# Optimization experiments

Hardware: AMD Instinct MI355X
Metric: run time of the kernel (lower is better)

## Reference

```python
import jax, jax.numpy as jnp
import numpy as np

V, E, H, L = 2048, 512, 1024, 2   # vocab, emb_dim, hidden, num_layers
NUM_LABELS = [50, 20, 10]
S, T = 1024, 512                   # encoder seq len, max_out_char_seq_len


def _gru_layer(xs, h0, wih, whh, bih, bhh):
    # torch GRU cell: r,z,n gate order. xs: (T, Din), h0: (H,)
    def step(h, x):
        gx = x @ wih.T + bih
        gh = h @ whh.T + bhh
        xr, xz, xn = jnp.split(gx, 3)
        hr, hz, hn = jnp.split(gh, 3)
        r = jax.nn.sigmoid(xr + hr)
        z = jax.nn.sigmoid(xz + hz)
        n = jnp.tanh(xn + r * hn)
        h_new = (1.0 - z) * n + z * h
        return h_new, h_new
    hT, hs = jax.lax.scan(step, h0, xs)
    return hs, hT


def _gru(xs, h0, params):
    # params: list of (wih, whh, bih, bhh) per layer; h0: (L, H)
    outs, finals = [], []
    inp = xs
    for l, (wih, whh, bih, bhh) in enumerate(params):
        hs, hT = _gru_layer(inp, h0[l], wih, whh, bih, bhh)
        outs.append(hs)
        finals.append(hT)
        inp = hs
    return outs, jnp.stack(finals)


def _forward(char_seq, target_char_seq, enc_state, emb,
             enc_wih0, enc_whh0, enc_bih0, enc_bhh0,
             enc_wih1, enc_whh1, enc_bih1, enc_bhh1,
             dec_wih0, dec_whh0, dec_bih0, dec_bhh0,
             dec_wih1, dec_whh1, dec_bih1, dec_bhh1,
             out_w, out_b, cls_w0, cls_b0, cls_w1, cls_b1, cls_w2, cls_b2,
             sos, max_out_char_seq_len, max_num_labels):
    enc_params = [(enc_wih0, enc_whh0, enc_bih0, enc_bhh0),
                  (enc_wih1, enc_whh1, enc_bih1, enc_bhh1)]
    dec_params = [(dec_wih0, dec_whh0, dec_bih0, dec_bhh0),
                  (dec_wih1, dec_whh1, dec_bih1, dec_bhh1)]
    # encode_: mask = char_seq != 0 is all-True by construction (inputs drawn from [4, V))
    _, h_enc = _gru(emb[char_seq], enc_state.reshape(L, H), enc_params)
    # teacher-forced decode: step t consumes <s> for t=0 else target[t-1];
    # targets contain no eos/sep, so the loop runs exactly max_out_char_seq_len steps
    dec_in = jnp.concatenate([jnp.asarray([sos], dtype=target_char_seq.dtype),
                              target_char_seq[: max_out_char_seq_len - 1]])
    layer_hs, _ = _gru(emb[dec_in], h_enc, dec_params)
    # char_dropout is identity in eval mode
    char_scores = layer_hs[-1] @ out_w.T + out_b            # (T, H) -- char_out_size == hidden
    char_scores_out = char_scores[None]                      # (1, T, H), no padding (full-length decode)
    # per-step stacked layer states, view(1, -1, L*H) layout == layer-major concat
    char_states_out = jnp.stack(layer_hs, axis=1).reshape(1, max_out_char_seq_len, L * H)
    # final decoder_label_step_ on last char_scores; padded to max_num_labels
    last = char_scores[-1]
    labels = []
    for w, b in ((cls_w0, cls_b0), (cls_w1, cls_b1), (cls_w2, cls_b2)):
        s = last @ w.T + b                                   # (num,)
        labels.append(jnp.pad(s[None, None, :], ((0, 0), (0, max_num_labels - 1), (0, 0))))
    return (char_scores_out, char_states_out, labels[0], labels[1], labels[2])


def setup_inputs() -> dict:
    key = jax.random.key(0)
    ks = list(jax.random.split(key, 40))
    nrm = lambda k, sh: jax.random.normal(k, sh, dtype=jnp.float32) * 0.05
    inp = {}
    inp["char_seq"] = jax.random.randint(ks[0], (S,), 4, V)       # avoid pad/sos/eos/sep ids
    inp["target_char_seq"] = jax.random.randint(ks[1], (T,), 4, V)
    inp["enc_state"] = nrm(ks[2], (L * H,))
    inp["emb"] = nrm(ks[3], (V, E))
    i = 4
    for pre in ("enc", "dec"):
        for l in range(L):
            din = E if l == 0 else H
            inp[f"{pre}_wih{l}"] = nrm(ks[i], (3 * H, din)); i += 1
            inp[f"{pre}_whh{l}"] = nrm(ks[i], (3 * H, H)); i += 1
            inp[f"{pre}_bih{l}"] = nrm(ks[i], (3 * H,)); i += 1
            inp[f"{pre}_bhh{l}"] = nrm(ks[i], (3 * H,)); i += 1
    inp["out_w"] = nrm(ks[i], (H, H)); i += 1
    inp["out_b"] = nrm(ks[i], (H,)); i += 1
    for j, n in enumerate(NUM_LABELS):
        inp[f"cls_w{j}"] = nrm(ks[i], (n, H)); i += 1
        inp[f"cls_b{j}"] = nrm(ks[i], (n,)); i += 1
    inp["sos"] = 1
    inp["max_out_char_seq_len"] = T
    inp["max_num_labels"] = 3
    return inp


def reference(char_seq, target_char_seq, enc_state, emb,
              enc_wih0, enc_whh0, enc_bih0, enc_bhh0,
              enc_wih1, enc_whh1, enc_bih1, enc_bhh1,
              dec_wih0, dec_whh0, dec_bih0, dec_bhh0,
              dec_wih1, dec_whh1, dec_bih1, dec_bhh1,
              out_w, out_b, cls_w0, cls_b0, cls_w1, cls_b1, cls_w2, cls_b2,
              sos, max_out_char_seq_len, max_num_labels):
    return _forward(char_seq, target_char_seq, enc_state, emb,
                    enc_wih0, enc_whh0, enc_bih0, enc_bhh0,
                    enc_wih1, enc_whh1, enc_bih1, enc_bhh1,
                    dec_wih0, dec_whh0, dec_bih0, dec_bhh0,
                    dec_wih1, dec_whh1, dec_bih1, dec_bhh1,
                    out_w, out_b, cls_w0, cls_b0, cls_w1, cls_b1, cls_w2, cls_b2,
                    sos, max_out_char_seq_len, max_num_labels)
```

## Files before the change

### kernel.cpp

```cpp
#include <hip/hip_runtime.h>
#include <hip/hip_bf16.h>
#include <cstdint>

#define Hh   1024
#define G3   3072
#define POISON_U 0xFFFFFFFFu

__device__ __forceinline__ float sigmoidf_(float x) { return 1.f / (1.f + __expf(-x)); }

__device__ __forceinline__ float ld_agent(const float* p) {
    return __hip_atomic_load(p, __ATOMIC_RELAXED, __HIP_MEMORY_SCOPE_AGENT);
}
__device__ __forceinline__ void st_agent(float* p, float v) {
    __hip_atomic_store(p, v, __ATOMIC_RELAXED, __HIP_MEMORY_SCOPE_AGENT);
}
__device__ __forceinline__ float poll_val(const float* p) {
    float v = ld_agent(p);
    int guard = 0;
    while (__float_as_uint(v) == POISON_U) {
        __builtin_amdgcn_s_sleep(1);
        v = ld_agent(p);
        if (++guard > (1 << 20)) break;
    }
    return v;
}

__global__ __launch_bounds__(128) void gather_emb(const int* __restrict__ char_seq,
    const int* __restrict__ target, const int* __restrict__ sos,
    const float* __restrict__ emb, float* __restrict__ x_enc, float* __restrict__ x_dec)
{
    const int r = blockIdx.x;
    int id; float* dst;
    if (r < 1024) { id = char_seq[r]; dst = x_enc + (size_t)r * 512; }
    else {
        const int rd = r - 1024;
        id = (rd == 0) ? sos[0] : target[rd - 1];
        dst = x_dec + (size_t)rd * 512;
    }
    const float4* src = (const float4*)(emb + (size_t)id * 512);
    ((float4*)dst)[threadIdx.x] = src[threadIdx.x];
}

__global__ __launch_bounds__(256) void gemm_nt(const float* __restrict__ A,
    const float* __restrict__ W, const float* __restrict__ bias,
    float* __restrict__ C, int M, int N, int K)
{
    __shared__ float As[16][68];
    __shared__ float Ws[16][68];
    const int tid = threadIdx.x;
    const int tx = tid & 15, ty = tid >> 4;
    const int row0 = blockIdx.y * 64, col0 = blockIdx.x * 64;
    const int lr = tid >> 2;
    const int ls = (tid & 3) << 2;
    float acc[4][4] = {};
    for (int k0 = 0; k0 < K; k0 += 16) {
        const float4 a4 = *(const float4*)(A + (size_t)(row0 + lr) * K + k0 + ls);
        const float4 w4 = *(const float4*)(W + (size_t)(col0 + lr) * K + k0 + ls);
        As[ls + 0][lr] = a4.x; As[ls + 1][lr] = a4.y; As[ls + 2][lr] = a4.z; As[ls + 3][lr] = a4.w;
        Ws[ls + 0][lr] = w4.x; Ws[ls + 1][lr] = w4.y; Ws[ls + 2][lr] = w4.z; Ws[ls + 3][lr] = w4.w;
        __syncthreads();
        #pragma unroll
        for (int k = 0; k < 16; ++k) {
            const float4 a = *(const float4*)&As[k][ty << 2];
            const float4 w = *(const float4*)&Ws[k][tx << 2];
            const float av[4] = {a.x, a.y, a.z, a.w};
            const float wv[4] = {w.x, w.y, w.z, w.w};
            #pragma unroll
            for (int i = 0; i < 4; ++i)
                #pragma unroll
                for (int j = 0; j < 4; ++j)
                    acc[i][j] += av[i] * wv[j];
        }
        __syncthreads();
    }
    const int cc = col0 + (tx << 2);
    #pragma unroll
    for (int i = 0; i < 4; ++i) {
        float4 o;
        o.x = acc[i][0] + bias[cc + 0];
        o.y = acc[i][1] + bias[cc + 1];
        o.z = acc[i][2] + bias[cc + 2];
        o.w = acc[i][3] + bias[cc + 3];
        *(float4*)(C + (size_t)(row0 + (ty << 2) + i) * N + cc) = o;
    }
}

__global__ __launch_bounds__(512, 2) void fused_gru2(
    const float* __restrict__ gx0,
    const float* __restrict__ whh0, const float* __restrict__ bhh0,
    const float* __restrict__ wih1, const float* __restrict__ bih1,
    const float* __restrict__ whh1, const float* __restrict__ bhh1,
    const float* __restrict__ h0i, const float* __restrict__ h1i,
    float* __restrict__ hs0, float* __restrict__ hs1, int S)
{
    __shared__ float sh0[Hh];
    __shared__ float sh1[Hh];
    const int tid = threadIdx.x;
    const int wg  = blockIdx.x;
    const bool isL1 = (wg >= 128);
    const int ln = tid & 63;
    const int wv = tid >> 6;
    const int uu = ((isL1 ? wg - 128 : wg) << 3) + wv;

    float4 wa[3][4], wb[3][4];
    const float* WA = isL1 ? wih1 : whh0;
    #pragma unroll
    for (int g = 0; g < 3; ++g)
        #pragma unroll
        for (int j = 0; j < 4; ++j)
            wa[g][j] = *(const float4*)(WA + (size_t)(g * Hh + uu) * Hh + ((ln + 64 * j) << 2));
    if (isL1) {
        #pragma unroll
        for (int g = 0; g < 3; ++g)
            #pragma unroll
            for (int j = 0; j < 4; ++j)
                wb[g][j] = *(const float4*)(whh1 + (size_t)(g * Hh + uu) * Hh + ((ln + 64 * j) << 2));
    } else {
        #pragma unroll
        for (int g = 0; g < 3; ++g)
            #pragma unroll
            for (int j = 0; j < 4; ++j)
                wb[g][j] = make_float4(0.f, 0.f, 0.f, 0.f);
    }
    const float* BA = isL1 ? bih1 : bhh0;
    const float ba_r = BA[uu], ba_z = BA[Hh + uu], ba_n = BA[2 * Hh + uu];
    const float bb_r = isL1 ? bhh1[uu] : 0.f;
    const float bb_z = isL1 ? bhh1[Hh + uu] : 0.f;
    const float bb_n = isL1 ? bhh1[2 * Hh + uu] : 0.f;

    const float4* s0f4 = (const float4*)sh0;
    const float4* s1f4 = (const float4*)sh1;

    for (int t = 0; t < S; ++t) {
        float xr = 0.f, xz = 0.f, xn = 0.f;
        if (!isL1 && ln == 0) {
            const float* gxt = gx0 + (size_t)t * G3 + uu;
            xr = gxt[0]; xz = gxt[Hh]; xn = gxt[2 * Hh];
        }

        if (!isL1) {
            if (t == 0) {
                sh0[tid] = h0i[tid]; sh0[tid + 512] = h0i[tid + 512];
            } else {
                const float* row = hs0 + (size_t)t * Hh;
                const float v0 = poll_val(&row[tid]);
                const float v1 = poll_val(&row[tid + 512]);
                sh0[tid] = v0; sh0[tid + 512] = v1;
            }
        } else {
            const float* rx = hs0 + (size_t)(t + 1) * Hh;
            const float v0 = poll_val(&rx[tid]);
            const float v1 = poll_val(&rx[tid + 512]);
            sh0[tid] = v0; sh0[tid + 512] = v1;
            if (t == 0) {
                sh1[tid] = h1i[tid]; sh1[tid + 512] = h1i[tid + 512];
            } else {
                const float* rh = hs1 + (size_t)t * Hh;
                const float w0 = poll_val(&rh[tid]);
                const float w1 = poll_val(&rh[tid + 512]);
                sh1[tid] = w0; sh1[tid + 512] = w1;
            }
        }
        __syncthreads();

        float ar = 0.f, az = 0.f, an = 0.f;
        float hr = 0.f, hz = 0.f, hn = 0.f;
        #pragma unroll
        for (int j = 0; j < 4; ++j) {
            const float4 x4 = s0f4[ln + 64 * j];
            ar += x4.x * wa[0][j].x + x4.y * wa[0][j].y + x4.z * wa[0][j].z + x4.w * wa[0][j].w;
            az += x4.x * wa[1][j].x + x4.y * wa[1][j].y + x4.z * wa[1][j].z + x4.w * wa[1][j].w;
            an += x4.x * wa[2][j].x + x4.y * wa[2][j].y + x4.z * wa[2][j].z + x4.w * wa[2][j].w;
        }
        if (isL1) {
            #pragma unroll
            for (int j = 0; j < 4; ++j) {
                const float4 h4 = s1f4[ln + 64 * j];
                hr += h4.x * wb[0][j].x + h4.y * wb[0][j].y + h4.z * wb[0][j].z + h4.w * wb[0][j].w;
                hz += h4.x * wb[1][j].x + h4.y * wb[1][j].y + h4.z * wb[1][j].z + h4.w * wb[1][j].w;
                hn += h4.x * wb[2][j].x + h4.y * wb[2][j].y + h4.z * wb[2][j].z + h4.w * wb[2][j].w;
            }
        }
        #pragma unroll
        for (int m = 1; m < 64; m <<= 1) {
            ar += __shfl_xor(ar, m); az += __shfl_xor(az, m); an += __shfl_xor(an, m);
            if (isL1) { hr += __shfl_xor(hr, m); hz += __shfl_xor(hz, m); hn += __shfl_xor(hn, m); }
        }
        if (ln == 0) {
            float rr, zz, nn, hprev;
            if (!isL1) {
                rr = sigmoidf_(xr + ar + ba_r);
                zz = sigmoidf_(xz + az + ba_z);
                nn = tanhf(xn + rr * (an + ba_n));
                hprev = sh0[uu];
            } else {
                rr = sigmoidf_((ar + ba_r) + (hr + bb_r));
                zz = sigmoidf_((az + ba_z) + (hz + bb_z));
                nn = tanhf((an + ba_n) + rr * (hn + bb_n));
                hprev = sh1[uu];
            }
            const float hnew = (1.f - zz) * nn + zz * hprev;
            st_agent((isL1 ? hs1 : hs0) + (size_t)(t + 1) * Hh + uu, hnew);
        }
        __syncthreads();
    }
}

__global__ __launch_bounds__(256) void copy_states(const float* __restrict__ hs0,
    const float* __restrict__ hs1, float* __restrict__ out)
{
    const int f = blockIdx.x * 256 + threadIdx.x;
    const int t = f >> 9;
    const int c = f & 511;
    const float* src = (c < 256) ? (hs0 + (((size_t)t + 1) << 10) + (c << 2))
                                 : (hs1 + (((size_t)t + 1) << 10) + ((c - 256) << 2));
    *(float4*)(out + ((size_t)f << 2)) = *(const float4*)src;
}

__global__ __launch_bounds__(256) void labels_kernel(const float* __restrict__ scores,
    const float* __restrict__ w0, const float* __restrict__ b0,
    const float* __restrict__ w1, const float* __restrict__ b1,
    const float* __restrict__ w2, const float* __restrict__ b2,
    float* __restrict__ out)
{
    __shared__ float sl[Hh];
    const int tid = threadIdx.x;
    for (int i = tid; i < Hh; i += 256) sl[i] = scores[(size_t)511 * Hh + i];
    for (int i = tid; i < 240; i += 256) out[i] = 0.f;
    __syncthreads();
    const int wv = tid >> 6, ln = tid & 63;
    for (int o = wv; o < 80; o += 4) {
        const float* w; float bb; float* dst;
        if (o < 50)      { w = w0 + (size_t)o * Hh;        bb = b0[o];      dst = out + o; }
        else if (o < 70) { w = w1 + (size_t)(o - 50) * Hh; bb = b1[o - 50]; dst = out + 150 + (o - 50); }
        else             { w = w2 + (size_t)(o - 70) * Hh; bb = b2[o - 70]; dst = out + 210 + (o - 70); }
        float s = 0.f;
        #pragma unroll
        for (int i = 0; i < 4; ++i) {
            const int k = (ln << 2) + (i << 8);
            const float4 ww = *(const float4*)&w[k];
            const float4 l4 = *(const float4*)&sl[k];
            s += ww.x * l4.x + ww.y * l4.y + ww.z * l4.z + ww.w * l4.w;
        }
        #pragma unroll
        for (int m = 1; m < 64; m <<= 1) s += __shfl_xor(s, m);
        if (ln == 0) *dst = s + bb;
    }
}

extern "C" void kernel_launch(void* const* d_in, const int* in_sizes, int n_in,
                              void* d_out, int out_size, void* d_ws, size_t ws_size,
                              hipStream_t stream)
{
    (void)in_sizes; (void)n_in; (void)out_size; (void)ws_size;
    const int*   char_seq  = (const int*)d_in[0];
    const int*   target    = (const int*)d_in[1];
    const float* enc_state = (const float*)d_in[2];
    const float* emb       = (const float*)d_in[3];
    const float* enc_wih0  = (const float*)d_in[4];
    const float* enc_whh0  = (const float*)d_in[5];
    const float* enc_bih0  = (const float*)d_in[6];
    const float* enc_bhh0  = (const float*)d_in[7];
    const float* enc_wih1  = (const float*)d_in[8];
    const float* enc_whh1  = (const float*)d_in[9];
    const float* enc_bih1  = (const float*)d_in[10];
    const float* enc_bhh1  = (const float*)d_in[11];
    const float* dec_wih0  = (const float*)d_in[12];
    const float* dec_whh0  = (const float*)d_in[13];
    const float* dec_bih0  = (const float*)d_in[14];
    const float* dec_bhh0  = (const float*)d_in[15];
    const float* dec_wih1  = (const float*)d_in[16];
    const float* dec_whh1  = (const float*)d_in[17];
    const float* dec_bih1  = (const float*)d_in[18];
    const float* dec_bhh1  = (const float*)d_in[19];
    const float* out_w     = (const float*)d_in[20];
    const float* out_b     = (const float*)d_in[21];
    const float* cls_w0    = (const float*)d_in[22];
    const float* cls_b0    = (const float*)d_in[23];
    const float* cls_w1    = (const float*)d_in[24];
    const float* cls_b1    = (const float*)d_in[25];
    const float* cls_w2    = (const float*)d_in[26];
    const float* cls_b2    = (const float*)d_in[27];
    const int*   sos       = (const int*)d_in[28];

    float* ws    = (float*)d_ws;
    float* x_enc = ws;
    float* x_dec = x_enc + 1024 * 512;
    float* gx    = x_dec + 512 * 512;
    float* hs_e0 = gx + 1024 * 3072;
    float* hs_e1 = hs_e0 + 1025 * 1024;
    float* hs_d0 = hs_e1 + 1025 * 1024;
    float* hs_d1 = hs_d0 + 513 * 1024;

    float* out        = (float*)d_out;
    float* out_scores = out;
    float* out_states = out + 512 * 1024;
    float* out_labels = out_states + 512 * 2048;

    hipMemsetAsync(hs_e0, 0xFF, (size_t)(1025 + 1025 + 513 + 513) * 1024 * sizeof(float), stream);

    gather_emb<<<1536, 128, 0, stream>>>(char_seq, target, sos, emb, x_enc, x_dec);

    gemm_nt<<<dim3(48, 16), 256, 0, stream>>>(x_enc, enc_wih0, enc_bih0, gx, 1024, 3072, 512);
    fused_gru2<<<256, 512, 0, stream>>>(gx, enc_whh0, enc_bhh0,
                                        enc_wih1, enc_bih1, enc_whh1, enc_bhh1,
                                        enc_state, enc_state + 1024,
                                        hs_e0, hs_e1, 1024);

    gemm_nt<<<dim3(48, 8), 256, 0, stream>>>(x_dec, dec_wih0, dec_bih0, gx, 512, 3072, 512);
    fused_gru2<<<256, 512, 0, stream>>>(gx, dec_whh0, dec_bhh0,
                                        dec_wih1, dec_bih1, dec_whh1, dec_bhh1,
                                        hs_e0 + 1024 * 1024, hs_e1 + 1024 * 1024,
                                        hs_d0, hs_d1, 512);

    gemm_nt<<<dim3(16, 8), 256, 0, stream>>>(hs_d1 + 1024, out_w, out_b, out_scores, 512, 1024, 1024);
    copy_states<<<1024, 256, 0, stream>>>(hs_d0, hs_d1, out_states);
    labels_kernel<<<1, 256, 0, stream>>>(out_scores, cls_w0, cls_b0, cls_w1, cls_b1, cls_w2, cls_b2, out_labels);
}
```

Baseline: 4.258 ms.

## Double-buffer shared state and vectorize polling in fused GRU recurrence

The per-step shared-memory hidden-state buffers become double-buffered by step parity, which allows the trailing __syncthreads in each timestep to be dropped. Polling of the hidden states written by other workgroups now reads four floats per thread instead of one, and the L1 workgroups divide the hs0 and hs1 polls across the two halves of the block so they run concurrently. The launch-bounds occupancy hint is removed and the gx loads are made unconditional. The aim is to cut per-step synchronisation and polling latency in the serial recurrence, at the cost of more shared memory and a dependence on the parity buffer preventing write-after-read hazards.

New measurement: 5.468 ms. +28.4%, slower.

```diff
diff --git a/kernel.cpp b/kernel.cpp
--- a/kernel.cpp
+++ b/kernel.cpp
@@ -14,13 +14,17 @@
 __device__ __forceinline__ void st_agent(float* p, float v) {
     __hip_atomic_store(p, v, __ATOMIC_RELAXED, __HIP_MEMORY_SCOPE_AGENT);
 }
-__device__ __forceinline__ float poll_val(const float* p) {
-    float v = ld_agent(p);
+__device__ __forceinline__ bool okf(float v) { return __float_as_uint(v) != POISON_U; }
+
+__device__ __forceinline__ float4 poll4(const float* p) {
+    float4 v;
     int guard = 0;
-    while (__float_as_uint(v) == POISON_U) {
+    for (;;) {
+        v.x = ld_agent(p + 0); v.y = ld_agent(p + 1);
+        v.z = ld_agent(p + 2); v.w = ld_agent(p + 3);
+        if (okf(v.x) && okf(v.y) && okf(v.z) && okf(v.w)) break;
+        if (++guard > (1 << 20)) break;
         __builtin_amdgcn_s_sleep(1);
-        v = ld_agent(p);
-        if (++guard > (1 << 20)) break;
     }
     return v;
 }
@@ -85,7 +89,7 @@
     }
 }
 
-__global__ __launch_bounds__(512, 2) void fused_gru2(
+__global__ __launch_bounds__(512) void fused_gru2(
     const float* __restrict__ gx0,
     const float* __restrict__ whh0, const float* __restrict__ bhh0,
     const float* __restrict__ wih1, const float* __restrict__ bih1,
@@ -93,14 +97,15 @@
     const float* __restrict__ h0i, const float* __restrict__ h1i,
     float* __restrict__ hs0, float* __restrict__ hs1, int S)
 {
-    __shared__ float sh0[Hh];
-    __shared__ float sh1[Hh];
+    __shared__ float shA[2][Hh];
+    __shared__ float shB[2][Hh];
     const int tid = threadIdx.x;
     const int wg  = blockIdx.x;
     const bool isL1 = (wg >= 128);
     const int ln = tid & 63;
     const int wv = tid >> 6;
     const int uu = ((isL1 ? wg - 128 : wg) << 3) + wv;
+    const int base = ln << 2;
 
     float4 wa[3][4], wb[3][4];
     const float* WA = isL1 ? wih1 : whh0;
@@ -108,13 +113,13 @@
     for (int g = 0; g < 3; ++g)
         #pragma unroll
         for (int j = 0; j < 4; ++j)
-            wa[g][j] = *(const float4*)(WA + (size_t)(g * Hh + uu) * Hh + ((ln + 64 * j) << 2));
+            wa[g][j] = *(const float4*)(WA + (size_t)(g * Hh + uu) * Hh + base + (j << 8));
     if (isL1) {
         #pragma unroll
         for (int g = 0; g < 3; ++g)
             #pragma unroll
             for (int j = 0; j < 4; ++j)
-                wb[g][j] = *(const float4*)(whh1 + (size_t)(g * Hh + uu) * Hh + ((ln + 64 * j) << 2));
+                wb[g][j] = *(const float4*)(whh1 + (size_t)(g * Hh + uu) * Hh + base + (j << 8));
     } else {
         #pragma unroll
         for (int g = 0; g < 3; ++g)
@@ -128,46 +133,43 @@
     const float bb_z = isL1 ? bhh1[Hh + uu] : 0.f;
     const float bb_n = isL1 ? bhh1[2 * Hh + uu] : 0.f;
 
-    const float4* s0f4 = (const float4*)sh0;
-    const float4* s1f4 = (const float4*)sh1;
-
     for (int t = 0; t < S; ++t) {
+        const int b = t & 1;
         float xr = 0.f, xz = 0.f, xn = 0.f;
-        if (!isL1 && ln == 0) {
+        if (!isL1) {
             const float* gxt = gx0 + (size_t)t * G3 + uu;
             xr = gxt[0]; xz = gxt[Hh]; xn = gxt[2 * Hh];
         }
 
         if (!isL1) {
-            if (t == 0) {
-                sh0[tid] = h0i[tid]; sh0[tid + 512] = h0i[tid + 512];
-            } else {
-                const float* row = hs0 + (size_t)t * Hh;
-                const float v0 = poll_val(&row[tid]);
-                const float v1 = poll_val(&row[tid + 512]);
-                sh0[tid] = v0; sh0[tid + 512] = v1;
+            if (tid < 256) {
+                const int off = tid << 2;
+                float4 v;
+                if (t == 0) v = *(const float4*)(h0i + off);
+                else        v = poll4(hs0 + (size_t)t * Hh + off);
+                *(float4*)&shA[b][off] = v;
             }
         } else {
-            const float* rx = hs0 + (size_t)(t + 1) * Hh;
-            const float v0 = poll_val(&rx[tid]);
-            const float v1 = poll_val(&rx[tid + 512]);
-            sh0[tid] = v0; sh0[tid + 512] = v1;
-            if (t == 0) {
-                sh1[tid] = h1i[tid]; sh1[tid + 512] = h1i[tid + 512];
+            if (tid < 256) {
+                const int off = tid << 2;
+                const float4 v = poll4(hs0 + (size_t)(t + 1) * Hh + off);
+                *(float4*)&shA[b][off] = v;
             } else {
-                const float* rh = hs1 + (size_t)t * Hh;
-                const float w0 = poll_val(&rh[tid]);
-                const float w1 = poll_val(&rh[tid + 512]);
-                sh1[tid] = w0; sh1[tid + 512] = w1;
+                const int off = (tid - 256) << 2;
+                float4 v;
+                if (t == 0) v = *(const float4*)(h1i + off);
+                else        v = poll4(hs1 + (size_t)t * Hh + off);
+                *(float4*)&shB[b][off] = v;
             }
         }
         __syncthreads();
 
-        float ar = 0.f, az = 0.f, an = 0.f;
-        float hr = 0.f, hz = 0.f, hn = 0.f;
+        const float4* sA = (const float4*)shA[b];
+        const float4* sB = (const float4*)shB[b];
+        float ar = 0.f, az = 0.f, an = 0.f, hr = 0.f, hz = 0.f, hn = 0.f;
         #pragma unroll
         for (int j = 0; j < 4; ++j) {
-            const float4 x4 = s0f4[ln + 64 * j];
+            const float4 x4 = sA[ln + 64 * j];
             ar += x4.x * wa[0][j].x + x4.y * wa[0][j].y + x4.z * wa[0][j].z + x4.w * wa[0][j].w;
             az += x4.x * wa[1][j].x + x4.y * wa[1][j].y + x4.z * wa[1][j].z + x4.w * wa[1][j].w;
             an += x4.x * wa[2][j].x + x4.y * wa[2][j].y + x4.z * wa[2][j].z + x4.w * wa[2][j].w;
@@ -175,7 +177,7 @@
         if (isL1) {
             #pragma unroll
             for (int j = 0; j < 4; ++j) {
-                const float4 h4 = s1f4[ln + 64 * j];
+                const float4 h4 = sB[ln + 64 * j];
                 hr += h4.x * wb[0][j].x + h4.y * wb[0][j].y + h4.z * wb[0][j].z + h4.w * wb[0][j].w;
                 hz += h4.x * wb[1][j].x + h4.y * wb[1][j].y + h4.z * wb[1][j].z + h4.w * wb[1][j].w;
                 hn += h4.x * wb[2][j].x + h4.y * wb[2][j].y + h4.z * wb[2][j].z + h4.w * wb[2][j].w;
@@ -192,17 +194,16 @@
                 rr = sigmoidf_(xr + ar + ba_r);
                 zz = sigmoidf_(xz + az + ba_z);
                 nn = tanhf(xn + rr * (an + ba_n));
-                hprev = sh0[uu];
+                hprev = shA[b][uu];
             } else {
                 rr = sigmoidf_((ar + ba_r) + (hr + bb_r));
                 zz = sigmoidf_((az + ba_z) + (hz + bb_z));
                 nn = tanhf((an + ba_n) + rr * (hn + bb_n));
-                hprev = sh1[uu];
+                hprev = shB[b][uu];
             }
             const float hnew = (1.f - zz) * nn + zz * hprev;
             st_agent((isL1 ? hs1 : hs0) + (size_t)(t + 1) * Hh + uu, hnew);
         }
-        __syncthreads();
     }
 }
 
```
